# Optimization experiments

Hardware: AMD Instinct MI355X
Metric: run time of the kernel (lower is better)

The kernel has to match this reference:

```python
import jax, jax.numpy as jnp
import numpy as np

B, S, HID = 4, 2048, 2048
NH, NKV, D = 16, 8, 128
RK, RV = 16, 16
HPG = NH // NKV
SCALING = D ** -0.5
NEG = -1e9


def _rope(x, cos, sin):
    # x: [B, S, H, D]; cos/sin: [S, D//2]. Gemma split-half complex rotation.
    x1, x2 = jnp.split(x, 2, axis=-1)
    c = cos[None, :, None, :]
    s = sin[None, :, None, :]
    return jnp.concatenate([x1 * c - x2 * s, x1 * s + x2 * c], axis=-1)


def setup_inputs() -> dict:
    key = jax.random.key(0)
    ks = jax.random.split(key, 8)
    hidden_states = jax.random.normal(ks[0], (B, S, HID), dtype=jnp.float32)
    # RoPE frequencies (theta=10000)
    inv_freq = 1.0 / (10000.0 ** (np.arange(0, D, 2, dtype=np.float32) / D))
    ang = np.arange(S, dtype=np.float32)[:, None] * inv_freq[None, :]
    freqs_cos = jnp.asarray(np.cos(ang), dtype=jnp.float32)
    freqs_sin = jnp.asarray(np.sin(ang), dtype=jnp.float32)
    kv_write_indices = jnp.arange(S, dtype=jnp.int32)
    # causal additive mask [1,1,S,S]
    causal = jnp.tril(jnp.ones((S, S), dtype=bool))
    mask = jnp.where(causal, 0.0, NEG).astype(jnp.float32)[None, None]
    sc = 0.02
    W_q = jax.random.normal(ks[1], (NH * D, HID), dtype=jnp.float32) * sc
    W_k = jax.random.normal(ks[2], (NKV * D, HID), dtype=jnp.float32) * sc
    W_v = jax.random.normal(ks[3], (NKV * D, HID), dtype=jnp.float32) * sc
    o_proj_w = jax.random.normal(ks[4], (HID, NH * D), dtype=jnp.float32) * sc
    V_r_basis = jax.random.normal(ks[5], (NH, D, RK), dtype=jnp.float32) * (D ** -0.5)
    Z_v_basis = jax.random.normal(ks[6], (NKV, D, RV), dtype=jnp.float32) * (D ** -0.5)
    return {"hidden_states": hidden_states, "freqs_cos": freqs_cos, "freqs_sin": freqs_sin,
            "kv_write_indices": kv_write_indices, "mask": mask, "W_q": W_q, "W_k": W_k,
            "W_v": W_v, "o_proj_w": o_proj_w, "V_r_basis": V_r_basis, "Z_v_basis": Z_v_basis}


def reference(hidden_states, freqs_cos, freqs_sin, kv_write_indices, mask,
              W_q, W_k, W_v, o_proj_w, V_r_basis, Z_v_basis):
    bsz, q_len, _ = hidden_states.shape
    q = (hidden_states @ W_q.T).reshape(bsz, q_len, NH, D)
    k = (hidden_states @ W_k.T).reshape(bsz, q_len, NKV, D)
    v = (hidden_states @ W_v.T).reshape(bsz, q_len, NKV, D)

    # project K per-head onto its group's basis (vectorized over the head loop)
    head_to_group = jnp.arange(NH) // HPG                       # [NH]
    k_per_head = k[:, :, head_to_group, :]                      # [B,S,NH,D]
    pk = jnp.einsum('bshd,hdr->bshr', k_per_head, V_r_basis)    # [B,S,NH,RK]
    pv = jnp.einsum('bqgd,gdr->bqgr', v, Z_v_basis)             # [B,S,NKV,RV]

    # factorized cache write (scatter along seq dim), prefill: kv_seq_len = S
    kv_seq_len = q_len
    cache_pk = jnp.zeros((bsz, kv_seq_len, NH, RK), hidden_states.dtype)
    cache_pv = jnp.zeros((bsz, kv_seq_len, NKV, RV), hidden_states.dtype)
    cache_pk = cache_pk.at[:, kv_write_indices].set(pk)
    cache_pv = cache_pv.at[:, kv_write_indices].set(pv)

    # reconstruct K/V from compressed cache
    k_hat = jnp.einsum('bshr,hrd->bshd', cache_pk, jnp.swapaxes(V_r_basis, -1, -2))
    v_hat = jnp.einsum('bsgr,grd->bsgd', cache_pv, jnp.swapaxes(Z_v_basis, -1, -2))

    # RoPE post-reconstruction
    q_rot = _rope(q, freqs_cos[:q_len], freqs_sin[:q_len])
    k_rot = _rope(k_hat, freqs_cos[:kv_seq_len], freqs_sin[:kv_seq_len])

    # GQA: repeat kv heads
    v_g = jnp.repeat(v_hat, HPG, axis=2)                        # [B,S,NH,D]

    scores = jnp.einsum('bqhd,bkhd->bhqk', q_rot, k_rot) * SCALING
    scores = scores + mask[:, :, :q_len, :kv_seq_len]
    probs = jax.nn.softmax(scores.astype(jnp.float32), axis=-1).astype(hidden_states.dtype)
    out = jnp.einsum('bhqk,bkhd->bqhd', probs, v_g)
    out = out.reshape(bsz, q_len, NH * D)
    return out @ o_proj_w.T
```

## Files before the change

kernel.cpp:

```cpp
#include <hip/hip_runtime.h>

typedef unsigned short ushort8 __attribute__((ext_vector_type(8)));
typedef short s16x8 __attribute__((ext_vector_type(8)));
typedef float f32x4 __attribute__((ext_vector_type(4)));

#define AS1 __attribute__((address_space(1)))
#define AS3 __attribute__((address_space(3)))

#define B_    4
#define S_    2048
#define HID_  2048
#define NH_   16
#define NKV_  8
#define D_    128
#define RK_   16
#define SCALING_ 0.08838834764831845f
#define NEGBIG   -1.0e30f

__device__ __forceinline__ float bf2f(unsigned short u) {
  union { unsigned int i; float f; } x; x.i = ((unsigned int)u) << 16; return x.f;
}
__device__ __forceinline__ unsigned short f2bf(float f) {
  union { float f; unsigned int i; } x; x.f = f;
  unsigned int r = x.i + 0x7fffu + ((x.i >> 16) & 1u);
  return (unsigned short)(r >> 16);
}

__global__ __launch_bounds__(256) void cvt_bf16(const float* __restrict__ in,
                                                unsigned short* __restrict__ out,
                                                int n8) {
  int i = blockIdx.x * 256 + threadIdx.x;
  const int stride = gridDim.x * 256;
  for (; i < n8; i += stride) {
    const float4 a = ((const float4*)in)[i * 2];
    const float4 b = ((const float4*)in)[i * 2 + 1];
    ushort8 u;
    u[0] = f2bf(a.x); u[1] = f2bf(a.y); u[2] = f2bf(a.z); u[3] = f2bf(a.w);
    u[4] = f2bf(b.x); u[5] = f2bf(b.y); u[6] = f2bf(b.z); u[7] = f2bf(b.w);
    *(ushort8*)&out[i * 8] = u;
  }
}

template<bool CBF>
__global__ __launch_bounds__(256) void gemm_mfma(const unsigned short* __restrict__ A,
                                                 const unsigned short* __restrict__ Bb,
                                                 void* __restrict__ C_,
                                                 int M, int N, int K) {
  __shared__ unsigned short Ash[128 * 64];
  __shared__ unsigned short Bsh[128 * 64];
  const int tid = threadIdx.x;
  const int w = tid >> 6, l = tid & 63, lg = l >> 4, ll = l & 15;
  const int wr = w >> 1, wc = w & 1;
  const int flat = blockIdx.y * gridDim.x + blockIdx.x;
  const int cpx = (gridDim.x * gridDim.y) >> 3;
  const int swz = (flat & 7) * cpx + (flat >> 3);
  const int bm = (swz / gridDim.x) * 128, bn = (swz % gridDim.x) * 128;

  f32x4 acc[4][4];
#pragma unroll
  for (int i = 0; i < 4; i++)
#pragma unroll
    for (int j = 0; j < 4; j++) acc[i][j] = (f32x4){0.f, 0.f, 0.f, 0.f};

  const int srow = tid >> 3;
  const int sslot = tid & 7;

  for (int k0 = 0; k0 < K; k0 += 64) {
    __syncthreads();
#pragma unroll
    for (int c = 0; c < 4; ++c) {
      const int row = c * 32 + srow;
      const int ss = sslot ^ (row & 7);
      const unsigned short* srcA = &A[(size_t)(bm + row) * K + k0 + ss * 8];
      const unsigned short* srcB = &Bb[(size_t)(bn + row) * K + k0 + ss * 8];
      char* dstA = ((char*)Ash) + c * 4096 + w * 1024;
      char* dstB = ((char*)Bsh) + c * 4096 + w * 1024;
      __builtin_amdgcn_global_load_lds((const AS1 void*)srcA, (AS3 void*)dstA, 16, 0, 0);
      __builtin_amdgcn_global_load_lds((const AS1 void*)srcB, (AS3 void*)dstB, 16, 0, 0);
    }
    __syncthreads();

#pragma unroll
    for (int ks = 0; ks < 2; ++ks) {
      s16x8 af[4], bf_[4];
#pragma unroll
      for (int mi = 0; mi < 4; ++mi) {
        const int row = wr * 64 + mi * 16 + ll;
        af[mi] = *(const s16x8*)&Ash[row * 64 + (((ks * 4 + lg) ^ (row & 7)) * 8)];
      }
#pragma unroll
      for (int ni = 0; ni < 4; ++ni) {
        const int row = wc * 64 + ni * 16 + ll;
        bf_[ni] = *(const s16x8*)&Bsh[row * 64 + (((ks * 4 + lg) ^ (row & 7)) * 8)];
      }
#pragma unroll
      for (int mi = 0; mi < 4; ++mi)
#pragma unroll
        for (int ni = 0; ni < 4; ++ni)
          acc[mi][ni] = __builtin_amdgcn_mfma_f32_16x16x32_bf16(af[mi], bf_[ni], acc[mi][ni], 0, 0, 0);
    }
  }

#pragma unroll
  for (int mi = 0; mi < 4; ++mi)
#pragma unroll
    for (int ni = 0; ni < 4; ++ni)
#pragma unroll
      for (int j = 0; j < 4; ++j) {
        const int row = bm + wr * 64 + mi * 16 + lg * 4 + j;
        const int col = bn + wc * 64 + ni * 16 + ll;
        if (CBF) ((unsigned short*)C_)[(size_t)row * N + col] = f2bf(acc[mi][ni][j]);
        else     ((float*)C_)[(size_t)row * N + col] = acc[mi][ni][j];
      }
}

__global__ __launch_bounds__(256) void rope_q(unsigned short* __restrict__ q,
                                              const float* __restrict__ cosT,
                                              const float* __restrict__ sinT) {
  const int p = blockIdx.x * 256 + threadIdx.x;
  const int d = p & 63;
  const int h = (p >> 6) & 15;
  const int s = (p >> 10) & 2047;
  const int b = p >> 21;
  const size_t base = (((size_t)b * S_ + s) * NH_ + h) * D_ + d;
  const float x1 = bf2f(q[base]), x2 = bf2f(q[base + 64]);
  const float c = cosT[s * 64 + d], sn = sinT[s * 64 + d];
  q[base]      = f2bf((x1 * c - x2 * sn) * SCALING_);
  q[base + 64] = f2bf((x1 * sn + x2 * c) * SCALING_);
}

__global__ __launch_bounds__(256) void pkpv_make(const unsigned short* __restrict__ k_raw,
                                                 const unsigned short* __restrict__ v_raw,
                                                 const float* __restrict__ Vr,
                                                 const float* __restrict__ Zv,
                                                 float* __restrict__ pk,
                                                 float* __restrict__ pv) {
  const int s = blockIdx.x, b = blockIdx.y;
  const int tid = threadIdx.x;
  __shared__ float kb[NKV_ * D_];
  __shared__ float vb[NKV_ * D_];
  {
    const size_t o = ((size_t)b * S_ + s) * (NKV_ * D_) + tid * 4;
    ushort4 ku = *(const ushort4*)&k_raw[o];
    kb[tid * 4 + 0] = bf2f(ku.x); kb[tid * 4 + 1] = bf2f(ku.y);
    kb[tid * 4 + 2] = bf2f(ku.z); kb[tid * 4 + 3] = bf2f(ku.w);
    ushort4 vu = *(const ushort4*)&v_raw[o];
    vb[tid * 4 + 0] = bf2f(vu.x); vb[tid * 4 + 1] = bf2f(vu.y);
    vb[tid * 4 + 2] = bf2f(vu.z); vb[tid * 4 + 3] = bf2f(vu.w);
  }
  __syncthreads();
  {
    const int h = tid >> 4, r = tid & 15, g = h >> 1;
    float a = 0.f;
    const float* vr = &Vr[(size_t)h * D_ * RK_ + r];
    const float* kk = &kb[g * D_];
#pragma unroll 8
    for (int d = 0; d < D_; d++) a += kk[d] * vr[d * RK_];
    pk[(((size_t)b * S_ + s) * NH_ + h) * RK_ + r] = a;
  }
  if (tid < 128) {
    const int g = tid >> 4, r = tid & 15;
    float a = 0.f;
    const float* zv = &Zv[(size_t)g * D_ * RK_ + r];
    const float* vv = &vb[g * D_];
#pragma unroll 8
    for (int d = 0; d < D_; d++) a += vv[d] * zv[d * RK_];
    pv[(((size_t)b * S_ + s) * NKV_ + g) * RK_ + r] = a;
  }
}

__global__ __launch_bounds__(256) void expand_k(const float* __restrict__ pk,
                                                const float* __restrict__ Vr,
                                                const float* __restrict__ cosT,
                                                const float* __restrict__ sinT,
                                                unsigned short* __restrict__ kr) {
  const int s0 = blockIdx.x * 32, h = blockIdx.y, b = blockIdx.z;
  const int tid = threadIdx.x;
  __shared__ float pkS[32][17];
  if (tid < 128) {
    const int r_ = tid >> 2, c4 = (tid & 3) * 4;
    float4 v = *(const float4*)&pk[(((size_t)b * S_ + s0 + r_) * NH_ + h) * RK_ + c4];
    pkS[r_][c4 + 0] = v.x; pkS[r_][c4 + 1] = v.y;
    pkS[r_][c4 + 2] = v.z; pkS[r_][c4 + 3] = v.w;
  }
  __syncthreads();
  const int row = tid >> 3, dl = tid & 7;
  float kh[16];
#pragma unroll
  for (int j = 0; j < 16; j++) {
    const int d = dl + 8 * j;
    const float4* w = (const float4*)&Vr[((size_t)h * D_ + d) * RK_];
    float a = 0.f;
#pragma unroll
    for (int q4 = 0; q4 < 4; q4++) {
      float4 wv = w[q4];
      a += pkS[row][q4 * 4 + 0] * wv.x + pkS[row][q4 * 4 + 1] * wv.y
         + pkS[row][q4 * 4 + 2] * wv.z + pkS[row][q4 * 4 + 3] * wv.w;
    }
    kh[j] = a;
  }
  const int pos = s0 + row;
  const size_t o = (((size_t)b * NH_ + h) * S_ + pos) * D_;
#pragma unroll
  for (int j = 0; j < 8; j++) {
    const int d = dl + 8 * j;
    const float c = cosT[pos * 64 + d], sn = sinT[pos * 64 + d];
    kr[o + d]      = f2bf(kh[j] * c - kh[j + 8] * sn);
    kr[o + d + 64] = f2bf(kh[j] * sn + kh[j + 8] * c);
  }
}

__global__ __launch_bounds__(256) void expand_v(const float* __restrict__ pv,
                                                const float* __restrict__ Zv,
                                                unsigned short* __restrict__ vh) {
  const int s0 = blockIdx.x * 32, g = blockIdx.y, b = blockIdx.z;
  const int tid = threadIdx.x;
  __shared__ float pvS[32][17];
  if (tid < 128) {
    const int r_ = tid >> 2, c4 = (tid & 3) * 4;
    float4 v = *(const float4*)&pv[(((size_t)b * S_ + s0 + r_) * NKV_ + g) * RK_ + c4];
    pvS[r_][c4 + 0] = v.x; pvS[r_][c4 + 1] = v.y;
    pvS[r_][c4 + 2] = v.z; pvS[r_][c4 + 3] = v.w;
  }
  __syncthreads();
  const int row = tid >> 3, dl = tid & 7;
  const size_t o = (((size_t)b * NKV_ + g) * S_ + s0 + row) * D_;
#pragma unroll
  for (int j = 0; j < 16; j++) {
    const int d = dl + 8 * j;
    const float4* w = (const float4*)&Zv[((size_t)g * D_ + d) * RK_];
    float a = 0.f;
#pragma unroll
    for (int q4 = 0; q4 < 4; q4++) {
      float4 wv = w[q4];
      a += pvS[row][q4 * 4 + 0] * wv.x + pvS[row][q4 * 4 + 1] * wv.y
         + pvS[row][q4 * 4 + 2] * wv.z + pvS[row][q4 * 4 + 3] * wv.w;
    }
    vh[o + d] = f2bf(a);
  }
}

__global__ __launch_bounds__(256) void attn_mfma(const unsigned short* __restrict__ q,
                                                 const unsigned short* __restrict__ kr,
                                                 const unsigned short* __restrict__ vh,
                                                 unsigned short* __restrict__ out) {
  const int flat = ((int)blockIdx.z * 16 + (int)blockIdx.y) * 16 + (int)blockIdx.x;
  const int swz = (flat & 7) * 128 + (flat >> 3);
  const int qt = 15 - (swz & 15);
  const int h = (swz >> 4) & 15;
  const int b = swz >> 8;
  const int g = h >> 1;
  const int tid = threadIdx.x;
  const int w = tid >> 6, l = tid & 63, lg = l >> 4, ll = l & 15;

  __shared__ unsigned short Klds[2][64 * 128];
  __shared__ unsigned short Vt[2][128 * 64];
  __shared__ unsigned short Ps[4][32 * 64];

  const int qr0 = qt * 128 + w * 32;
  const int ktmax = 2 * qt + 1;
  const int kmy = 2 * qt + (w >> 1);

  s16x8 qf[2][4];
#pragma unroll
  for (int mi = 0; mi < 2; ++mi)
#pragma unroll
    for (int ks = 0; ks < 4; ++ks)
      qf[mi][ks] = *(const s16x8*)&q[(((size_t)b * S_ + qr0 + mi * 16 + ll) * NH_ + h) * D_ + ks * 32 + lg * 8];

  f32x4 o[2][8];
#pragma unroll
  for (int mi = 0; mi < 2; ++mi)
#pragma unroll
    for (int nd = 0; nd < 8; ++nd) o[mi][nd] = (f32x4){0.f, 0.f, 0.f, 0.f};
  float m_[2][4], l_[2][4];
#pragma unroll
  for (int mi = 0; mi < 2; ++mi)
#pragma unroll
    for (int j = 0; j < 4; ++j) { m_[mi][j] = NEGBIG; l_[mi][j] = 0.f; }

  const unsigned short* kbase = &kr[(((size_t)b * NH_ + h) * S_) * D_];
  const unsigned short* vbase = &vh[(((size_t)b * NKV_ + g) * S_) * D_];
  const int vk = (tid & 31) * 2, d0v = (tid >> 5) * 16;

  ushort8 va0, va1, vb0, vb1;
  {
#pragma unroll
    for (int c = 0; c < 4; ++c) {
      const int ro = c * 16 + w * 4 + lg;
      const int ss = ll ^ (ro & 7);
      const unsigned short* src = kbase + ro * D_ + ss * 8;
      char* dst = ((char*)&Klds[0][0]) + c * 4096 + w * 1024;
      __builtin_amdgcn_global_load_lds((const AS1 void*)src, (AS3 void*)dst, 16, 0, 0);
    }
    const unsigned short* v0 = vbase + (size_t)vk * D_ + d0v;
    va0 = *(const ushort8*)v0; va1 = *(const ushort8*)(v0 + 8);
    vb0 = *(const ushort8*)(v0 + D_); vb1 = *(const ushort8*)(v0 + D_ + 8);
#pragma unroll
    for (int j = 0; j < 8; ++j) {
      const int d1 = d0v + j, d2 = d0v + 8 + j;
      *(unsigned int*)&Vt[0][d1 * 64 + (((vk >> 3) ^ (d1 & 7)) * 8) + (vk & 7)] =
          (unsigned int)va0[j] | ((unsigned int)vb0[j] << 16);
      *(unsigned int*)&Vt[0][d2 * 64 + (((vk >> 3) ^ (d2 & 7)) * 8) + (vk & 7)] =
          (unsigned int)va1[j] | ((unsigned int)vb1[j] << 16);
    }
  }
  __syncthreads();

  for (int kt = 0; kt <= ktmax; ++kt) {
    const int p = kt & 1;
    if (kt < ktmax) {
      const unsigned short* kb2 = kbase + (size_t)(kt + 1) * 64 * D_;
#pragma unroll
      for (int c = 0; c < 4; ++c) {
        const int ro = c * 16 + w * 4 + lg;
        const int ss = ll ^ (ro & 7);
        const unsigned short* src = kb2 + ro * D_ + ss * 8;
        char* dst = ((char*)&Klds[p ^ 1][0]) + c * 4096 + w * 1024;
        __builtin_amdgcn_global_load_lds((const AS1 void*)src, (AS3 void*)dst, 16, 0, 0);
      }
      const unsigned short* v0 = vbase + (size_t)((kt + 1) * 64 + vk) * D_ + d0v;
      va0 = *(const ushort8*)v0; va1 = *(const ushort8*)(v0 + 8);
      vb0 = *(const ushort8*)(v0 + D_); vb1 = *(const ushort8*)(v0 + D_ + 8);
    }

    if (kt <= kmy) {
      f32x4 s[2][4];
#pragma unroll
      for (int mi = 0; mi < 2; ++mi)
#pragma unroll
        for (int ni = 0; ni < 4; ++ni) s[mi][ni] = (f32x4){0.f, 0.f, 0.f, 0.f};
#pragma unroll
      for (int ks = 0; ks < 4; ++ks) {
#pragma unroll
        for (int ni = 0; ni < 4; ++ni) {
          const int row = ni * 16 + ll;
          const s16x8 kf = *(const s16x8*)&Klds[p][row * 128 + (((ks * 4 + lg) ^ (row & 7)) * 8)];
          s[0][ni] = __builtin_amdgcn_mfma_f32_16x16x32_bf16(qf[0][ks], kf, s[0][ni], 0, 0, 0);
          s[1][ni] = __builtin_amdgcn_mfma_f32_16x16x32_bf16(qf[1][ks], kf, s[1][ni], 0, 0, 0);
        }
      }

      const bool diag = (kt == kmy);
      float lm[2][4];
#pragma unroll
      for (int mi = 0; mi < 2; ++mi)
#pragma unroll
        for (int j = 0; j < 4; ++j) {
          if (diag) {
            const int qg = qr0 + mi * 16 + lg * 4 + j;
#pragma unroll
            for (int ni = 0; ni < 4; ++ni)
              if (kt * 64 + ni * 16 + ll > qg) s[mi][ni][j] = NEGBIG;
          }
          lm[mi][j] = fmaxf(fmaxf(s[mi][0][j], s[mi][1][j]),
                            fmaxf(s[mi][2][j], s[mi][3][j]));
        }
      float excess = lm[0][0] - m_[0][0];
#pragma unroll
      for (int mi = 0; mi < 2; ++mi)
#pragma unroll
        for (int j = 0; j < 4; ++j) excess = fmaxf(excess, lm[mi][j] - m_[mi][j]);
      const bool slow = __any(excess > 8.0f);

#pragma unroll
      for (int mi = 0; mi < 2; ++mi)
#pragma unroll
        for (int j = 0; j < 4; ++j) {
          float ps_[4];
          if (slow) {
            float mt = lm[mi][j];
            mt = fmaxf(mt, __shfl_xor(mt, 1));
            mt = fmaxf(mt, __shfl_xor(mt, 2));
            mt = fmaxf(mt, __shfl_xor(mt, 4));
            mt = fmaxf(mt, __shfl_xor(mt, 8));
            const float mnew = fmaxf(m_[mi][j], mt);
            const float al = __expf(m_[mi][j] - mnew);
            m_[mi][j] = mnew;
            float sum = 0.f;
#pragma unroll
            for (int ni = 0; ni < 4; ++ni) { ps_[ni] = __expf(s[mi][ni][j] - mnew); sum += ps_[ni]; }
            l_[mi][j] = l_[mi][j] * al + sum;
#pragma unroll
            for (int nd = 0; nd < 8; ++nd) o[mi][nd][j] *= al;
          } else {
            float sum = 0.f;
#pragma unroll
            for (int ni = 0; ni < 4; ++ni) { ps_[ni] = __expf(s[mi][ni][j] - m_[mi][j]); sum += ps_[ni]; }
            l_[mi][j] += sum;
          }
          const int prow = mi * 16 + lg * 4 + j;
#pragma unroll
          for (int nq = 0; nq < 2; ++nq) {
            unsigned int u;
            asm("v_cvt_pk_bf16_f32 %0, %1, %2" : "=v"(u) : "v"(ps_[nq * 2]), "v"(ps_[nq * 2 + 1]));
            const int c0 = nq * 32 + ll, c1 = nq * 32 + 16 + ll;
            Ps[w][prow * 64 + (((c0 >> 3) ^ (prow & 7)) * 8) + (ll & 7)] = (unsigned short)u;
            Ps[w][prow * 64 + (((c1 >> 3) ^ (prow & 7)) * 8) + (ll & 7)] = (unsigned short)(u >> 16);
          }
        }

      s16x8 pa[2][2];
#pragma unroll
      for (int mi = 0; mi < 2; ++mi)
#pragma unroll
        for (int ks2 = 0; ks2 < 2; ++ks2) {
          const int prow = mi * 16 + ll;
          pa[mi][ks2] = *(const s16x8*)&Ps[w][prow * 64 + (((ks2 * 4 + lg) ^ (prow & 7)) * 8)];
        }
#pragma unroll
      for (int nd = 0; nd < 8; ++nd) {
#pragma unroll
        for (int ks2 = 0; ks2 < 2; ++ks2) {
          const int vr = nd * 16 + ll;
          const s16x8 vbf = *(const s16x8*)&Vt[p][vr * 64 + (((ks2 * 4 + lg) ^ (vr & 7)) * 8)];
          o[0][nd] = __builtin_amdgcn_mfma_f32_16x16x32_bf16(pa[0][ks2], vbf, o[0][nd], 0, 0, 0);
          o[1][nd] = __builtin_amdgcn_mfma_f32_16x16x32_bf16(pa[1][ks2], vbf, o[1][nd], 0, 0, 0);
        }
      }
    }

    if (kt < ktmax) {
#pragma unroll
      for (int j = 0; j < 8; ++j) {
        const int d1 = d0v + j, d2 = d0v + 8 + j;
        *(unsigned int*)&Vt[p ^ 1][d1 * 64 + (((vk >> 3) ^ (d1 & 7)) * 8) + (vk & 7)] =
            (unsigned int)va0[j] | ((unsigned int)vb0[j] << 16);
        *(unsigned int*)&Vt[p ^ 1][d2 * 64 + (((vk >> 3) ^ (d2 & 7)) * 8) + (vk & 7)] =
            (unsigned int)va1[j] | ((unsigned int)vb1[j] << 16);
      }
    }
    __syncthreads();
  }

#pragma unroll
  for (int mi = 0; mi < 2; ++mi)
#pragma unroll
    for (int j = 0; j < 4; ++j) {
      float ls = l_[mi][j];
      ls += __shfl_xor(ls, 1);
      ls += __shfl_xor(ls, 2);
      ls += __shfl_xor(ls, 4);
      ls += __shfl_xor(ls, 8);
      const float inv = 1.f / ls;
      const size_t rowg = (size_t)b * S_ + qr0 + mi * 16 + lg * 4 + j;
      unsigned short* op = &out[rowg * (NH_ * D_) + h * D_ + ll];
#pragma unroll
      for (int nd = 0; nd < 8; ++nd) op[nd * 16] = f2bf(o[mi][nd][j] * inv);
    }
}

extern "C" void kernel_launch(void* const* d_in, const int* in_sizes, int n_in,
                              void* d_out, int out_size, void* d_ws, size_t ws_size,
                              hipStream_t stream) {
  const float* hidden = (const float*)d_in[0];
  const float* cosT   = (const float*)d_in[1];
  const float* sinT   = (const float*)d_in[2];
  const float* W_q    = (const float*)d_in[5];
  const float* W_k    = (const float*)d_in[6];
  const float* W_v    = (const float*)d_in[7];
  const float* W_o    = (const float*)d_in[8];
  const float* Vr     = (const float*)d_in[9];
  const float* Zv     = (const float*)d_in[10];
  float* out = (float*)d_out;

  char* ws = (char*)d_ws;
  unsigned short* hb     = (unsigned short*)(ws + 0);
  unsigned short* attn_b = (unsigned short*)(ws + 0);
  unsigned short* q_b    = (unsigned short*)(ws + 33554432);
  unsigned short* kraw_b = (unsigned short*)(ws + 67108864);
  unsigned short* vraw_b = (unsigned short*)(ws + 83886080);
  unsigned short* kr_b   = (unsigned short*)(ws + 67108864);
  unsigned short* vh_b   = (unsigned short*)(ws + 100663296);
  unsigned short* WR1    = (unsigned short*)(ws + 117440512);
  unsigned short* WR2    = (unsigned short*)(ws + 125829120);
  float*          pk_f   = (float*)(ws + 117440512);
  float*          pv_f   = (float*)(ws + 125829120);

  const int M = B_ * S_;

  cvt_bf16<<<2048, 256, 0, stream>>>(hidden, hb, (B_ * S_ * HID_) / 8);
  cvt_bf16<<<2048, 256, 0, stream>>>(W_q, WR1, (HID_ * HID_) / 8);
  cvt_bf16<<<2048, 256, 0, stream>>>(W_k, WR2, (NKV_ * D_ * HID_) / 8);

  gemm_mfma<true><<<dim3(16, 64), 256, 0, stream>>>(hb, WR1, q_b,    M, NH_ * D_,  HID_);
  gemm_mfma<true><<<dim3( 8, 64), 256, 0, stream>>>(hb, WR2, kraw_b, M, NKV_ * D_, HID_);
  cvt_bf16<<<2048, 256, 0, stream>>>(W_v, WR2, (NKV_ * D_ * HID_) / 8);
  gemm_mfma<true><<<dim3( 8, 64), 256, 0, stream>>>(hb, WR2, vraw_b, M, NKV_ * D_, HID_);

  rope_q<<<(B_ * S_ * NH_ * 64) / 256, 256, 0, stream>>>(q_b, cosT, sinT);

  pkpv_make<<<dim3(S_, B_), 256, 0, stream>>>(kraw_b, vraw_b, Vr, Zv, pk_f, pv_f);

  expand_k<<<dim3(S_ / 32, NH_, B_), 256, 0, stream>>>(pk_f, Vr, cosT, sinT, kr_b);
  expand_v<<<dim3(S_ / 32, NKV_, B_), 256, 0, stream>>>(pv_f, Zv, vh_b);

  cvt_bf16<<<2048, 256, 0, stream>>>(W_o, WR1, (HID_ * HID_) / 8);

  attn_mfma<<<dim3(16, 16, 4), 256, 0, stream>>>(q_b, kr_b, vh_b, attn_b);

  gemm_mfma<false><<<dim3(16, 64), 256, 0, stream>>>(attn_b, WR1, out, M, HID_, HID_);
}
```

Baseline: 832.8 us.

## Fuse K/V projection GEMMs, use 8-wave attention blocks, and switch softmax to exp2

K and V weights are converted into one concatenated buffer so a single GEMM with N=2048 produces both projections, and pkpv_make reads the interleaved result. The attention kernel moves from 4 waves handling 32 query rows each to 8 waves handling 16 rows each, with 512 threads per block and K/V tile loads split across more threads. Q is prescaled by log2(e) so the softmax uses exp2f, and the lazy-rescale threshold is raised to match. s_setprio is placed around the MFMA sections. Per-wave work shrinks and register pressure drops, at the cost of each wave reusing K/V tiles across fewer query rows and a larger block that needs more synchronisation.

```diff
diff --git a/kernel.cpp b/kernel.cpp
--- a/kernel.cpp
+++ b/kernel.cpp
@@ -15,6 +15,7 @@
 #define D_    128
 #define RK_   16
 #define SCALING_ 0.08838834764831845f
+#define LOG2E_   1.4426950408889634f
 #define NEGBIG   -1.0e30f
 
 __device__ __forceinline__ float bf2f(unsigned short u) {
@@ -125,12 +126,12 @@
   const size_t base = (((size_t)b * S_ + s) * NH_ + h) * D_ + d;
   const float x1 = bf2f(q[base]), x2 = bf2f(q[base + 64]);
   const float c = cosT[s * 64 + d], sn = sinT[s * 64 + d];
-  q[base]      = f2bf((x1 * c - x2 * sn) * SCALING_);
-  q[base + 64] = f2bf((x1 * sn + x2 * c) * SCALING_);
-}
-
-__global__ __launch_bounds__(256) void pkpv_make(const unsigned short* __restrict__ k_raw,
-                                                 const unsigned short* __restrict__ v_raw,
+  const float sc = SCALING_ * LOG2E_;
+  q[base]      = f2bf((x1 * c - x2 * sn) * sc);
+  q[base + 64] = f2bf((x1 * sn + x2 * c) * sc);
+}
+
+__global__ __launch_bounds__(256) void pkpv_make(const unsigned short* __restrict__ kv_raw,
                                                  const float* __restrict__ Vr,
                                                  const float* __restrict__ Zv,
                                                  float* __restrict__ pk,
@@ -140,11 +141,11 @@
   __shared__ float kb[NKV_ * D_];
   __shared__ float vb[NKV_ * D_];
   {
-    const size_t o = ((size_t)b * S_ + s) * (NKV_ * D_) + tid * 4;
-    ushort4 ku = *(const ushort4*)&k_raw[o];
+    const size_t o = ((size_t)b * S_ + s) * 2048;
+    ushort4 ku = *(const ushort4*)&kv_raw[o + tid * 4];
     kb[tid * 4 + 0] = bf2f(ku.x); kb[tid * 4 + 1] = bf2f(ku.y);
     kb[tid * 4 + 2] = bf2f(ku.z); kb[tid * 4 + 3] = bf2f(ku.w);
-    ushort4 vu = *(const ushort4*)&v_raw[o];
+    ushort4 vu = *(const ushort4*)&kv_raw[o + 1024 + tid * 4];
     vb[tid * 4 + 0] = bf2f(vu.x); vb[tid * 4 + 1] = bf2f(vu.y);
     vb[tid * 4 + 2] = bf2f(vu.z); vb[tid * 4 + 3] = bf2f(vu.w);
   }
@@ -240,10 +241,10 @@
   }
 }
 
-__global__ __launch_bounds__(256) void attn_mfma(const unsigned short* __restrict__ q,
-                                                 const unsigned short* __restrict__ kr,
-                                                 const unsigned short* __restrict__ vh,
-                                                 unsigned short* __restrict__ out) {
+__global__ __launch_bounds__(512, 4) void attn_mfma(const unsigned short* __restrict__ q,
+                                                    const unsigned short* __restrict__ kr,
+                                                    const unsigned short* __restrict__ vh,
+                                                    unsigned short* __restrict__ out) {
   const int flat = ((int)blockIdx.z * 16 + (int)blockIdx.y) * 16 + (int)blockIdx.x;
   const int swz = (flat & 7) * 128 + (flat >> 3);
   const int qt = 15 - (swz & 15);
@@ -255,54 +256,46 @@
 
   __shared__ unsigned short Klds[2][64 * 128];
   __shared__ unsigned short Vt[2][128 * 64];
-  __shared__ unsigned short Ps[4][32 * 64];
-
-  const int qr0 = qt * 128 + w * 32;
+  __shared__ unsigned short Ps[8][16 * 64];
+
+  const int qr0 = qt * 128 + w * 16;
   const int ktmax = 2 * qt + 1;
-  const int kmy = 2 * qt + (w >> 1);
-
-  s16x8 qf[2][4];
-#pragma unroll
-  for (int mi = 0; mi < 2; ++mi)
-#pragma unroll
-    for (int ks = 0; ks < 4; ++ks)
-      qf[mi][ks] = *(const s16x8*)&q[(((size_t)b * S_ + qr0 + mi * 16 + ll) * NH_ + h) * D_ + ks * 32 + lg * 8];
-
-  f32x4 o[2][8];
-#pragma unroll
-  for (int mi = 0; mi < 2; ++mi)
-#pragma unroll
-    for (int nd = 0; nd < 8; ++nd) o[mi][nd] = (f32x4){0.f, 0.f, 0.f, 0.f};
-  float m_[2][4], l_[2][4];
-#pragma unroll
-  for (int mi = 0; mi < 2; ++mi)
-#pragma unroll
-    for (int j = 0; j < 4; ++j) { m_[mi][j] = NEGBIG; l_[mi][j] = 0.f; }
+  const int kmy = 2 * qt + (w >> 2);
+
+  s16x8 qf[4];
+#pragma unroll
+  for (int ks = 0; ks < 4; ++ks)
+    qf[ks] = *(const s16x8*)&q[(((size_t)b * S_ + qr0 + ll) * NH_ + h) * D_ + ks * 32 + lg * 8];
+
+  f32x4 o[8];
+#pragma unroll
+  for (int nd = 0; nd < 8; ++nd) o[nd] = (f32x4){0.f, 0.f, 0.f, 0.f};
+  float m_[4], l_[4];
+#pragma unroll
+  for (int j = 0; j < 4; ++j) { m_[j] = NEGBIG; l_[j] = 0.f; }
 
   const unsigned short* kbase = &kr[(((size_t)b * NH_ + h) * S_) * D_];
   const unsigned short* vbase = &vh[(((size_t)b * NKV_ + g) * S_) * D_];
-  const int vk = (tid & 31) * 2, d0v = (tid >> 5) * 16;
-
-  ushort8 va0, va1, vb0, vb1;
+  const int vk = (tid & 31) * 2;
+  const int vd0 = (tid >> 5) * 8;
+
+  ushort8 va, vb2;
   {
 #pragma unroll
-    for (int c = 0; c < 4; ++c) {
-      const int ro = c * 16 + w * 4 + lg;
-      const int ss = ll ^ (ro & 7);
-      const unsigned short* src = kbase + ro * D_ + ss * 8;
-      char* dst = ((char*)&Klds[0][0]) + c * 4096 + w * 1024;
+    for (int c = 0; c < 2; ++c) {
+      const int row = c * 32 + (tid >> 4);
+      const int ss = (tid & 15) ^ (row & 7);
+      const unsigned short* src = kbase + row * D_ + ss * 8;
+      char* dst = ((char*)&Klds[0][0]) + c * 8192 + w * 1024;
       __builtin_amdgcn_global_load_lds((const AS1 void*)src, (AS3 void*)dst, 16, 0, 0);
     }
-    const unsigned short* v0 = vbase + (size_t)vk * D_ + d0v;
-    va0 = *(const ushort8*)v0; va1 = *(const ushort8*)(v0 + 8);
-    vb0 = *(const ushort8*)(v0 + D_); vb1 = *(const ushort8*)(v0 + D_ + 8);
+    const unsigned short* v0 = vbase + (size_t)vk * D_ + vd0;
+    va = *(const ushort8*)v0; vb2 = *(const ushort8*)(v0 + D_);
 #pragma unroll
     for (int j = 0; j < 8; ++j) {
-      const int d1 = d0v + j, d2 = d0v + 8 + j;
-      *(unsigned int*)&Vt[0][d1 * 64 + (((vk >> 3) ^ (d1 & 7)) * 8) + (vk & 7)] =
-          (unsigned int)va0[j] | ((unsigned int)vb0[j] << 16);
-      *(unsigned int*)&Vt[0][d2 * 64 + (((vk >> 3) ^ (d2 & 7)) * 8) + (vk & 7)] =
-          (unsigned int)va1[j] | ((unsigned int)vb1[j] << 16);
+      const int d = vd0 + j;
+      *(unsigned int*)&Vt[0][d * 64 + (((vk >> 3) ^ (d & 7)) * 8) + (vk & 7)] =
+          (unsigned int)va[j] | ((unsigned int)vb2[j] << 16);
     }
   }
   __syncthreads();
@@ -312,142 +305,126 @@
     if (kt < ktmax) {
       const unsigned short* kb2 = kbase + (size_t)(kt + 1) * 64 * D_;
 #pragma unroll
-      for (int c = 0; c < 4; ++c) {
-        const int ro = c * 16 + w * 4 + lg;
-        const int ss = ll ^ (ro & 7);
-        const unsigned short* src = kb2 + ro * D_ + ss * 8;
-        char* dst = ((char*)&Klds[p ^ 1][0]) + c * 4096 + w * 1024;
+      for (int c = 0; c < 2; ++c) {
+        const int row = c * 32 + (tid >> 4);
+        const int ss = (tid & 15) ^ (row & 7);
+        const unsigned short* src = kb2 + row * D_ + ss * 8;
+        char* dst = ((char*)&Klds[p ^ 1][0]) + c * 8192 + w * 1024;
         __builtin_amdgcn_global_load_lds((const AS1 void*)src, (AS3 void*)dst, 16, 0, 0);
       }
-      const unsigned short* v0 = vbase + (size_t)((kt + 1) * 64 + vk) * D_ + d0v;
-      va0 = *(const ushort8*)v0; va1 = *(const ushort8*)(v0 + 8);
-      vb0 = *(const ushort8*)(v0 + D_); vb1 = *(const ushort8*)(v0 + D_ + 8);
+      const unsigned short* v0 = vbase + (size_t)((kt + 1) * 64 + vk) * D_ + vd0;
+      va = *(const ushort8*)v0; vb2 = *(const ushort8*)(v0 + D_);
     }
 
     if (kt <= kmy) {
-      f32x4 s[2][4];
-#pragma unroll
-      for (int mi = 0; mi < 2; ++mi)
-#pragma unroll
-        for (int ni = 0; ni < 4; ++ni) s[mi][ni] = (f32x4){0.f, 0.f, 0.f, 0.f};
+      f32x4 s[4];
+#pragma unroll
+      for (int ni = 0; ni < 4; ++ni) s[ni] = (f32x4){0.f, 0.f, 0.f, 0.f};
+      __builtin_amdgcn_s_setprio(1);
 #pragma unroll
       for (int ks = 0; ks < 4; ++ks) {
 #pragma unroll
         for (int ni = 0; ni < 4; ++ni) {
           const int row = ni * 16 + ll;
           const s16x8 kf = *(const s16x8*)&Klds[p][row * 128 + (((ks * 4 + lg) ^ (row & 7)) * 8)];
-          s[0][ni] = __builtin_amdgcn_mfma_f32_16x16x32_bf16(qf[0][ks], kf, s[0][ni], 0, 0, 0);
-          s[1][ni] = __builtin_amdgcn_mfma_f32_16x16x32_bf16(qf[1][ks], kf, s[1][ni], 0, 0, 0);
+          s[ni] = __builtin_amdgcn_mfma_f32_16x16x32_bf16(qf[ks], kf, s[ni], 0, 0, 0);
         }
       }
+      __builtin_amdgcn_s_setprio(0);
 
       const bool diag = (kt == kmy);
-      float lm[2][4];
-#pragma unroll
-      for (int mi = 0; mi < 2; ++mi)
-#pragma unroll
-        for (int j = 0; j < 4; ++j) {
-          if (diag) {
-            const int qg = qr0 + mi * 16 + lg * 4 + j;
-#pragma unroll
-            for (int ni = 0; ni < 4; ++ni)
-              if (kt * 64 + ni * 16 + ll > qg) s[mi][ni][j] = NEGBIG;
-          }
-          lm[mi][j] = fmaxf(fmaxf(s[mi][0][j], s[mi][1][j]),
-                            fmaxf(s[mi][2][j], s[mi][3][j]));
+      float lm[4];
+#pragma unroll
+      for (int j = 0; j < 4; ++j) {
+        if (diag) {
+          const int qg = qr0 + lg * 4 + j;
+#pragma unroll
+          for (int ni = 0; ni < 4; ++ni)
+            if (kt * 64 + ni * 16 + ll > qg) s[ni][j] = NEGBIG;
         }
-      float excess = lm[0][0] - m_[0][0];
-#pragma unroll
-      for (int mi = 0; mi < 2; ++mi)
-#pragma unroll
-        for (int j = 0; j < 4; ++j) excess = fmaxf(excess, lm[mi][j] - m_[mi][j]);
-      const bool slow = __any(excess > 8.0f);
-
-#pragma unroll
-      for (int mi = 0; mi < 2; ++mi)
-#pragma unroll
-        for (int j = 0; j < 4; ++j) {
-          float ps_[4];
-          if (slow) {
-            float mt = lm[mi][j];
-            mt = fmaxf(mt, __shfl_xor(mt, 1));
-            mt = fmaxf(mt, __shfl_xor(mt, 2));
-            mt = fmaxf(mt, __shfl_xor(mt, 4));
-            mt = fmaxf(mt, __shfl_xor(mt, 8));
-            const float mnew = fmaxf(m_[mi][j], mt);
-            const float al = __expf(m_[mi][j] - mnew);
-            m_[mi][j] = mnew;
-            float sum = 0.f;
-#pragma unroll
-            for (int ni = 0; ni < 4; ++ni) { ps_[ni] = __expf(s[mi][ni][j] - mnew); sum += ps_[ni]; }
-            l_[mi][j] = l_[mi][j] * al + sum;
-#pragma unroll
-            for (int nd = 0; nd < 8; ++nd) o[mi][nd][j] *= al;
-          } else {
-            float sum = 0.f;
-#pragma unroll
-            for (int ni = 0; ni < 4; ++ni) { ps_[ni] = __expf(s[mi][ni][j] - m_[mi][j]); sum += ps_[ni]; }
-            l_[mi][j] += sum;
-          }
-          const int prow = mi * 16 + lg * 4 + j;
-#pragma unroll
-          for (int nq = 0; nq < 2; ++nq) {
-            unsigned int u;
-            asm("v_cvt_pk_bf16_f32 %0, %1, %2" : "=v"(u) : "v"(ps_[nq * 2]), "v"(ps_[nq * 2 + 1]));
-            const int c0 = nq * 32 + ll, c1 = nq * 32 + 16 + ll;
-            Ps[w][prow * 64 + (((c0 >> 3) ^ (prow & 7)) * 8) + (ll & 7)] = (unsigned short)u;
-            Ps[w][prow * 64 + (((c1 >> 3) ^ (prow & 7)) * 8) + (ll & 7)] = (unsigned short)(u >> 16);
-          }
+        lm[j] = fmaxf(fmaxf(s[0][j], s[1][j]), fmaxf(s[2][j], s[3][j]));
+      }
+      float excess = lm[0] - m_[0];
+#pragma unroll
+      for (int j = 1; j < 4; ++j) excess = fmaxf(excess, lm[j] - m_[j]);
+      const bool slow = __any(excess > 11.5f);
+
+#pragma unroll
+      for (int j = 0; j < 4; ++j) {
+        float ps_[4];
+        if (slow) {
+          float mt = lm[j];
+          mt = fmaxf(mt, __shfl_xor(mt, 1));
+          mt = fmaxf(mt, __shfl_xor(mt, 2));
+          mt = fmaxf(mt, __shfl_xor(mt, 4));
+          mt = fmaxf(mt, __shfl_xor(mt, 8));
+          const float mnew = fmaxf(m_[j], mt);
+          const float al = exp2f(m_[j] - mnew);
+          m_[j] = mnew;
+          float sum = 0.f;
+#pragma unroll
+          for (int ni = 0; ni < 4; ++ni) { ps_[ni] = exp2f(s[ni][j] - mnew); sum += ps_[ni]; }
+          l_[j] = l_[j] * al + sum;
+#pragma unroll
+          for (int nd = 0; nd < 8; ++nd) o[nd][j] *= al;
+        } else {
+          float sum = 0.f;
+#pragma unroll
+          for (int ni = 0; ni < 4; ++ni) { ps_[ni] = exp2f(s[ni][j] - m_[j]); sum += ps_[ni]; }
+          l_[j] += sum;
         }
-
-      s16x8 pa[2][2];
-#pragma unroll
-      for (int mi = 0; mi < 2; ++mi)
-#pragma unroll
-        for (int ks2 = 0; ks2 < 2; ++ks2) {
-          const int prow = mi * 16 + ll;
-          pa[mi][ks2] = *(const s16x8*)&Ps[w][prow * 64 + (((ks2 * 4 + lg) ^ (prow & 7)) * 8)];
+        const int prow = lg * 4 + j;
+#pragma unroll
+        for (int nq = 0; nq < 2; ++nq) {
+          unsigned int u;
+          asm("v_cvt_pk_bf16_f32 %0, %1, %2" : "=v"(u) : "v"(ps_[nq * 2]), "v"(ps_[nq * 2 + 1]));
+          const int c0 = nq * 32 + ll, c1 = nq * 32 + 16 + ll;
+          Ps[w][prow * 64 + (((c0 >> 3) ^ (prow & 7)) * 8) + (ll & 7)] = (unsigned short)u;
+          Ps[w][prow * 64 + (((c1 >> 3) ^ (prow & 7)) * 8) + (ll & 7)] = (unsigned short)(u >> 16);
         }
+      }
+
+      s16x8 pa[2];
+#pragma unroll
+      for (int ks2 = 0; ks2 < 2; ++ks2)
+        pa[ks2] = *(const s16x8*)&Ps[w][ll * 64 + (((ks2 * 4 + lg) ^ (ll & 7)) * 8)];
+      __builtin_amdgcn_s_setprio(1);
 #pragma unroll
       for (int nd = 0; nd < 8; ++nd) {
 #pragma unroll
         for (int ks2 = 0; ks2 < 2; ++ks2) {
           const int vr = nd * 16 + ll;
           const s16x8 vbf = *(const s16x8*)&Vt[p][vr * 64 + (((ks2 * 4 + lg) ^ (vr & 7)) * 8)];
-          o[0][nd] = __builtin_amdgcn_mfma_f32_16x16x32_bf16(pa[0][ks2], vbf, o[0][nd], 0, 0, 0);
-          o[1][nd] = __builtin_amdgcn_mfma_f32_16x16x32_bf16(pa[1][ks2], vbf, o[1][nd], 0, 0, 0);
+          o[nd] = __builtin_amdgcn_mfma_f32_16x16x32_bf16(pa[ks2], vbf, o[nd], 0, 0, 0);
         }
       }
+      __builtin_amdgcn_s_setprio(0);
     }
 
     if (kt < ktmax) {
 #pragma unroll
       for (int j = 0; j < 8; ++j) {
-        const int d1 = d0v + j, d2 = d0v + 8 + j;
-        *(unsigned int*)&Vt[p ^ 1][d1 * 64 + (((vk >> 3) ^ (d1 & 7)) * 8) + (vk & 7)] =
-            (unsigned int)va0[j] | ((unsigned int)vb0[j] << 16);
-        *(unsigned int*)&Vt[p ^ 1][d2 * 64 + (((vk >> 3) ^ (d2 & 7)) * 8) + (vk & 7)] =
-            (unsigned int)va1[j] | ((unsigned int)vb1[j] << 16);
+        const int d = vd0 + j;
+        *(unsigned int*)&Vt[p ^ 1][d * 64 + (((vk >> 3) ^ (d & 7)) * 8) + (vk & 7)] =
+            (unsigned int)va[j] | ((unsigned int)vb2[j] << 16);
       }
     }
     __syncthreads();
   }
 
 #pragma unroll
-  for (int mi = 0; mi < 2; ++mi)
-#pragma unroll
-    for (int j = 0; j < 4; ++j) {
-      float ls = l_[mi][j];
-      ls += __shfl_xor(ls, 1);
-      ls += __shfl_xor(ls, 2);
-      ls += __shfl_xor(ls, 4);
-      ls += __shfl_xor(ls, 8);
-      const float inv = 1.f / ls;
-      const size_t rowg = (size_t)b * S_ + qr0 + mi * 16 + lg * 4 + j;
-      unsigned short* op = &out[rowg * (NH_ * D_) + h * D_ + ll];
-#pragma unroll
-      for (int nd = 0; nd < 8; ++nd) op[nd * 16] = f2bf(o[mi][nd][j] * inv);
-    }
+  for (int j = 0; j < 4; ++j) {
+    float ls = l_[j];
+    ls += __shfl_xor(ls, 1);
+    ls += __shfl_xor(ls, 2);
+    ls += __shfl_xor(ls, 4);
+    ls += __shfl_xor(ls, 8);
+    const float inv = 1.f / ls;
+    const size_t rowg = (size_t)b * S_ + qr0 + lg * 4 + j;
+    unsigned short* op = &out[rowg * (NH_ * D_) + h * D_ + ll];
+#pragma unroll
+    for (int nd = 0; nd < 8; ++nd) op[nd * 16] = f2bf(o[nd][j] * inv);
+  }
 }
 
 extern "C" void kernel_launch(void* const* d_in, const int* in_sizes, int n_in,
@@ -468,12 +445,11 @@
   unsigned short* hb     = (unsigned short*)(ws + 0);
   unsigned short* attn_b = (unsigned short*)(ws + 0);
   unsigned short* q_b    = (unsigned short*)(ws + 33554432);
-  unsigned short* kraw_b = (unsigned short*)(ws + 67108864);
-  unsigned short* vraw_b = (unsigned short*)(ws + 83886080);
+  unsigned short* kv_b   = (unsigned short*)(ws + 67108864);
   unsigned short* kr_b   = (unsigned short*)(ws + 67108864);
   unsigned short* vh_b   = (unsigned short*)(ws + 100663296);
+  unsigned short* Wkv    = (unsigned short*)(ws + 100663296);
   unsigned short* WR1    = (unsigned short*)(ws + 117440512);
-  unsigned short* WR2    = (unsigned short*)(ws + 125829120);
   float*          pk_f   = (float*)(ws + 117440512);
   float*          pv_f   = (float*)(ws + 125829120);
 
@@ -481,23 +457,22 @@
 
   cvt_bf16<<<2048, 256, 0, stream>>>(hidden, hb, (B_ * S_ * HID_) / 8);
   cvt_bf16<<<2048, 256, 0, stream>>>(W_q, WR1, (HID_ * HID_) / 8);
-  cvt_bf16<<<2048, 256, 0, stream>>>(W_k, WR2, (NKV_ * D_ * HID_) / 8);
-
-  gemm_mfma<true><<<dim3(16, 64), 256, 0, stream>>>(hb, WR1, q_b,    M, NH_ * D_,  HID_);
-  gemm_mfma<true><<<dim3( 8, 64), 256, 0, stream>>>(hb, WR2, kraw_b, M, NKV_ * D_, HID_);
-  cvt_bf16<<<2048, 256, 0, stream>>>(W_v, WR2, (NKV_ * D_ * HID_) / 8);
-  gemm_mfma<true><<<dim3( 8, 64), 256, 0, stream>>>(hb, WR2, vraw_b, M, NKV_ * D_, HID_);
+  cvt_bf16<<<1024, 256, 0, stream>>>(W_k, Wkv, (NKV_ * D_ * HID_) / 8);
+  cvt_bf16<<<1024, 256, 0, stream>>>(W_v, Wkv + (size_t)NKV_ * D_ * HID_, (NKV_ * D_ * HID_) / 8);
+
+  gemm_mfma<true><<<dim3(16, 64), 256, 0, stream>>>(hb, WR1, q_b,  M, 2048, HID_);
+  gemm_mfma<true><<<dim3(16, 64), 256, 0, stream>>>(hb, Wkv, kv_b, M, 2048, HID_);
 
   rope_q<<<(B_ * S_ * NH_ * 64) / 256, 256, 0, stream>>>(q_b, cosT, sinT);
 
-  pkpv_make<<<dim3(S_, B_), 256, 0, stream>>>(kraw_b, vraw_b, Vr, Zv, pk_f, pv_f);
+  pkpv_make<<<dim3(S_, B_), 256, 0, stream>>>(kv_b, Vr, Zv, pk_f, pv_f);
 
   expand_k<<<dim3(S_ / 32, NH_, B_), 256, 0, stream>>>(pk_f, Vr, cosT, sinT, kr_b);
   expand_v<<<dim3(S_ / 32, NKV_, B_), 256, 0, stream>>>(pv_f, Zv, vh_b);
 
   cvt_bf16<<<2048, 256, 0, stream>>>(W_o, WR1, (HID_ * HID_) / 8);
 
-  attn_mfma<<<dim3(16, 16, 4), 256, 0, stream>>>(q_b, kr_b, vh_b, attn_b);
+  attn_mfma<<<dim3(16, 16, 4), 512, 0, stream>>>(q_b, kr_b, vh_b, attn_b);
 
   gemm_mfma<false><<<dim3(16, 64), 256, 0, stream>>>(attn_b, WR1, out, M, HID_, HID_);
 }
```

New measurement: 998.9 us. 1.2x slower.
